# Performance work log

Measured on AMD Instinct MI355X. Metric: run time of the kernel, lower is better.

## Reference

```python
import jax, jax.numpy as jnp
import numpy as np

H = 1024          # hidden_size
NH = 16           # num_attention_heads
HD = H // NH      # head_size
EPS = 1e-5


def setup_inputs() -> dict:
    key = jax.random.key(0)
    ks = jax.random.split(key, 5)
    # xavier_uniform bound for Linear(in, out): sqrt(6/(in+out))
    b_qkv = float(np.sqrt(6.0 / (H + 3 * H)))
    b_out = float(np.sqrt(6.0 / (H + H)))
    return {
        "hidden_states": jax.random.normal(ks[0], (2, 2048, H), dtype=jnp.float32),
        "ln_gamma": jnp.ones((H,), jnp.float32),
        "ln_beta": jnp.zeros((H,), jnp.float32),
        "W_qkv": jax.random.uniform(ks[1], (3 * H, H), jnp.float32, -b_qkv, b_qkv),
        "b_qkv": jnp.zeros((3 * H,), jnp.float32),
        "W_out": jax.random.uniform(ks[2], (H, H), jnp.float32, -b_out, b_out),
        "b_out": jnp.zeros((H,), jnp.float32),
    }


def _attn_block(x, ln_gamma, ln_beta, W_qkv, b_qkv, W_out, b_out):
    B, S, _ = x.shape
    # Pre-LN
    mu = jnp.mean(x, axis=-1, keepdims=True)
    var = jnp.mean(jnp.square(x - mu), axis=-1, keepdims=True)
    xn = (x - mu) / jnp.sqrt(var + EPS) * ln_gamma + ln_beta
    # fused QKV projection: [B,S,3H]
    qkv = jnp.einsum("bsh,oh->bso", xn, W_qkv) + b_qkv
    qkv = qkv.reshape(B, S, 3, NH, HD).transpose(2, 0, 3, 1, 4)  # [3,B,NH,S,HD]
    q, k, v = qkv[0], qkv[1], qkv[2]
    scores = jnp.einsum("bhqd,bhkd->bhqk", q, k) / jnp.sqrt(jnp.asarray(HD, x.dtype))
    probs = jax.nn.softmax(scores, axis=-1)
    ctx = jnp.einsum("bhqk,bhkd->bhqd", probs, v)
    ctx = ctx.transpose(0, 2, 1, 3).reshape(B, S, H)
    out = jnp.einsum("bsh,oh->bso", ctx, W_out) + b_out  # dropout: eval mode = identity
    return x + out


def reference(hidden_states, ln_gamma, ln_beta, W_qkv, b_qkv, W_out, b_out):
    return _attn_block(hidden_states, ln_gamma, ln_beta, W_qkv, b_qkv, W_out, b_out)
```

## Files before the change

kernel.cpp:

```cpp
#include <hip/hip_runtime.h>
#include <stdint.h>

typedef unsigned short u16;
typedef __attribute__((ext_vector_type(8))) short bf16x8;
typedef __attribute__((ext_vector_type(4))) float f32x4;
typedef __attribute__((ext_vector_type(16))) float f32x16;
typedef __attribute__((ext_vector_type(4))) unsigned int u32x4;
typedef __attribute__((ext_vector_type(2))) unsigned int u32x2;
typedef __attribute__((ext_vector_type(4))) unsigned short u16x4;

#define QSCALE 0.18033688011112042f

typedef __attribute__((address_space(1))) const void gvoid;
typedef __attribute__((address_space(3))) void svoid;

__device__ __forceinline__ void cp16(const u16* g, u16* l) {
    __builtin_amdgcn_global_load_lds((gvoid*)g, (svoid*)l, 16, 0, 0);
}

__device__ __forceinline__ u16 f2bf(float f) {
    uint32_t u = __float_as_uint(f);
    u += 0x7fff + ((u >> 16) & 1);
    return (u16)(u >> 16);
}

__device__ __forceinline__ uint32_t pack_bf2(float lo, float hi) {
    uint32_t a = __float_as_uint(lo) + 0x8000u;
    uint32_t b = __float_as_uint(hi) + 0x8000u;
    return __builtin_amdgcn_perm(b, a, 0x07060302);
}

__device__ __forceinline__ f32x16 zero16() {
    f32x16 v;
    #pragma unroll
    for (int i = 0; i < 16; i++) v[i] = 0.f;
    return v;
}

__global__ __launch_bounds__(256) void k_pre(const float* __restrict__ X,
                                             const float* __restrict__ gam,
                                             const float* __restrict__ bet,
                                             u16* __restrict__ XN,
                                             const float* __restrict__ Wqkv, u16* __restrict__ Wq,
                                             const float* __restrict__ Wout, u16* __restrict__ Wo) {
    __shared__ float red[8];
    const int bid = blockIdx.x;
    if (bid < 4096) {
        int t = bid;
        const float4* xp = (const float4*)(X + (size_t)t * 1024);
        float4 x = xp[threadIdx.x];
        float s  = x.x + x.y + x.z + x.w;
        float s2 = x.x*x.x + x.y*x.y + x.z*x.z + x.w*x.w;
        #pragma unroll
        for (int off = 1; off < 64; off <<= 1) {
            s  += __shfl_xor(s,  off, 64);
            s2 += __shfl_xor(s2, off, 64);
        }
        int lane = threadIdx.x & 63, w = threadIdx.x >> 6;
        if (lane == 0) { red[w] = s; red[w + 4] = s2; }
        __syncthreads();
        s  = red[0] + red[1] + red[2] + red[3];
        s2 = red[4] + red[5] + red[6] + red[7];
        float mu  = s * (1.0f / 1024.0f);
        float var = s2 * (1.0f / 1024.0f) - mu * mu;
        float rin = rsqrtf(var + 1e-5f);
        float4 g = ((const float4*)gam)[threadIdx.x];
        float4 b = ((const float4*)bet)[threadIdx.x];
        u16x4 o;
        o.x = f2bf((x.x - mu) * rin * g.x + b.x);
        o.y = f2bf((x.y - mu) * rin * g.y + b.y);
        o.z = f2bf((x.z - mu) * rin * g.z + b.z);
        o.w = f2bf((x.w - mu) * rin * g.w + b.w);
        *(u16x4*)(XN + (size_t)t * 1024 + threadIdx.x * 4) = o;
    } else {
        int i = (bid - 4096) * 256 + threadIdx.x;
        const float* src; u16* dst;
        if (i < 786432) { src = Wqkv; dst = Wq; }
        else            { i -= 786432; src = Wout; dst = Wo; }
        float4 v = ((const float4*)src)[i];
        u16x4 o;
        o.x = f2bf(v.x); o.y = f2bf(v.y); o.z = f2bf(v.z); o.w = f2bf(v.w);
        ((u16x4*)dst)[i] = o;
    }
}

__device__ __forceinline__ void gemm_bt_tile(const u16* __restrict__ A, const u16* __restrict__ Bm,
                                             int m0, int n0, u16* As, u16* Bs, f32x4 acc[4][4]) {
    const int tid = threadIdx.x;
    const int lane = tid & 63;
    const int wv = tid >> 6;
    const int qi = lane & 15, g = lane >> 4, swz = qi & 7;
    const int wr = (wv >> 1) * 64, wc = (wv & 1) * 64;
    #pragma unroll
    for (int mi = 0; mi < 4; mi++)
        #pragma unroll
        for (int ni = 0; ni < 4; ni++) acc[mi][ni] = (f32x4){0.f, 0.f, 0.f, 0.f};

    const int row_in = tid >> 3;
    const int cs = (tid & 7) ^ (row_in & 7);
    for (int k0 = 0; k0 < 1024; k0 += 64) {
        __syncthreads();
        #pragma unroll
        for (int i = 0; i < 4; i++) {
            int row = i * 32 + row_in;
            cp16(A  + (size_t)(m0 + row) * 1024 + k0 + cs * 8, As + (i * 256 + wv * 64) * 8);
            cp16(Bm + (size_t)(n0 + row) * 1024 + k0 + cs * 8, Bs + (i * 256 + wv * 64) * 8);
        }
        __syncthreads();
        #pragma unroll
        for (int ks = 0; ks < 2; ks++) {
            bf16x8 af[4], bf[4];
            #pragma unroll
            for (int mi = 0; mi < 4; mi++)
                af[mi] = *(const bf16x8*)(As + (wr + mi * 16 + qi) * 64 + ((ks * 4 + g) ^ swz) * 8);
            #pragma unroll
            for (int ni = 0; ni < 4; ni++)
                bf[ni] = *(const bf16x8*)(Bs + (wc + ni * 16 + qi) * 64 + ((ks * 4 + g) ^ swz) * 8);
            #pragma unroll
            for (int mi = 0; mi < 4; mi++)
                #pragma unroll
                for (int ni = 0; ni < 4; ni++)
                    acc[mi][ni] = __builtin_amdgcn_mfma_f32_16x16x32_bf16(af[mi], bf[ni], acc[mi][ni], 0, 0, 0);
        }
    }
}


#define CFENCE asm volatile("" ::: "memory")
#define BARX() do { CFENCE; __builtin_amdgcn_s_barrier(); CFENCE; } while (0)
#define LGKM0() asm volatile("s_waitcnt lgkmcnt(0)" ::: "memory")

__global__ __launch_bounds__(512, 2) void k_qkv(const u16* __restrict__ XN, const u16* __restrict__ Wq,
                                                const float* __restrict__ bqkv,
                                                u16* __restrict__ Q, u16* __restrict__ K,
                                                u16* __restrict__ Vt) {
    __shared__ __align__(16) u16 SMEM[65536];
    const int tid = threadIdx.x;
    const int lane = tid & 63, w = tid >> 6;
    const int qi = lane & 15, g = lane >> 4, swz = qi & 7;
    const int wr = (w >> 2) * 128, wc = (w & 3) * 64;

    const int id = blockIdx.x;
    const int sw = (id & 7) * 24 + (id >> 3);
    const int n0 = (sw % 12) * 256;
    const int m0 = (sw / 12) * 256;

    const int laneRow = lane >> 3, laneCg = lane & 7;
    const int cs = laneCg ^ laneRow;
    const int aw = (w & 3) * 8 + (w >> 2) * 128;
    const u16* gA = XN + (size_t)(m0 + aw + laneRow) * 1024 + cs * 8;
    const u16* gB = Wq + (size_t)(n0 + w * 8 + laneRow) * 1024 + cs * 8;

#define SM_A(s) (SMEM + (s) * 32768)
#define SM_B(s) (SMEM + (s) * 32768 + 16384)
#define STAGE_A(tau, q, s) cp16(gA + (size_t)(q) * 32 * 1024 + (tau) * 64, SM_A(s) + ((q) * 32 + aw) * 64)
#define STAGE_B(tau, part, s)                                                                       \
    do { cp16(gB + (size_t)(part) * 128 * 1024 + (tau) * 64, SM_B(s) + ((part) * 128 + w * 8) * 64); \
         cp16(gB + (size_t)((part) * 128 + 64) * 1024 + (tau) * 64,                                  \
              SM_B(s) + ((part) * 128 + 64 + w * 8) * 64); } while (0)

    f32x4 acc[8][4];
    #pragma unroll
    for (int mi = 0; mi < 8; mi++)
        #pragma unroll
        for (int ni = 0; ni < 4; ni++) acc[mi][ni] = (f32x4){0.f, 0.f, 0.f, 0.f};
    bf16x8 bf[4][2];

    STAGE_B(0, 0, 0); STAGE_B(0, 1, 0);
    STAGE_A(0, 0, 0); STAGE_A(0, 1, 0); STAGE_A(0, 2, 0); STAGE_A(0, 3, 0);
    STAGE_B(1, 0, 1); STAGE_B(1, 1, 1);
    STAGE_A(1, 0, 1); STAGE_A(1, 1, 1);
    asm volatile("s_waitcnt vmcnt(6)" ::: "memory");
    BARX();

#define PHASE_A(q)                                                                                   \
    bf16x8 af[2][2];                                                                                 \
    _Pragma("unroll") for (int m2 = 0; m2 < 2; m2++)                                                 \
    _Pragma("unroll") for (int ks = 0; ks < 2; ks++)                                                 \
        af[m2][ks] = *(const bf16x8*)(as_ + (wr + ((q) * 2 + m2) * 16 + qi) * 64 + (((ks * 4 + g) ^ swz)) * 8);

#define DO_MFMA(q)                                                                                   \
    __builtin_amdgcn_s_setprio(1);                                                                   \
    _Pragma("unroll") for (int m2 = 0; m2 < 2; m2++)                                                 \
    _Pragma("unroll") for (int ni = 0; ni < 4; ni++) {                                               \
        acc[(q) * 2 + m2][ni] = __builtin_amdgcn_mfma_f32_16x16x32_bf16(af[m2][0], bf[ni][0], acc[(q) * 2 + m2][ni], 0, 0, 0); \
        acc[(q) * 2 + m2][ni] = __builtin_amdgcn_mfma_f32_16x16x32_bf16(af[m2][1], bf[ni][1], acc[(q) * 2 + m2][ni], 0, 0, 0); \
    }                                                                                                \
    __builtin_amdgcn_s_setprio(0);

    for (int t = 0; t < 16; t++) {
        const int s = t & 1;
        const u16* as_ = SM_A(s);
        const u16* bs_ = SM_B(s);
        {
            PHASE_A(0)
            #pragma unroll
            for (int ni = 0; ni < 4; ni++)
                #pragma unroll
                for (int ks = 0; ks < 2; ks++)
                    bf[ni][ks] = *(const bf16x8*)(bs_ + (wc + ni * 16 + qi) * 64 + ((ks * 4 + g) ^ swz) * 8);
            if (t < 15) { STAGE_A(t + 1, 2, s ^ 1); STAGE_A(t + 1, 3, s ^ 1); }
            BARX(); LGKM0();
            DO_MFMA(0)
            BARX();
        }
        {
            PHASE_A(1)
            if (t < 14) STAGE_B(t + 2, 0, s);
            BARX(); LGKM0();
            DO_MFMA(1)
            BARX();
        }
        {
            PHASE_A(2)
            if (t < 14) STAGE_B(t + 2, 1, s);
            BARX(); LGKM0();
            DO_MFMA(2)
            BARX();
        }
        {
            PHASE_A(3)
            if (t < 14) { STAGE_A(t + 2, 0, s); STAGE_A(t + 2, 1, s); }
            BARX(); LGKM0();
            DO_MFMA(3)
            if (t < 14) { asm volatile("s_waitcnt vmcnt(6)" ::: "memory"); }
            else        { asm volatile("s_waitcnt vmcnt(0)" ::: "memory"); }
            BARX();
        }
    }

    if (n0 < 2048) {
        const int which = n0 >> 10;
        u16* base = which ? K : Q;
        const float scale = which ? 1.0f : QSCALE;
        #pragma unroll
        for (int mi = 0; mi < 8; mi++)
            #pragma unroll
            for (int ni = 0; ni < 4; ni++)
                #pragma unroll
                for (int i = 0; i < 4; i++) {
                    int m = m0 + wr + mi * 16 + (g * 4 + i);
                    int n = n0 + wc + ni * 16 + qi;
                    float v = (acc[mi][ni][i] + bqkv[n]) * scale;
                    int b = m >> 11, ss = m & 2047;
                    int hh = (n >> 6) & 15, d = n & 63;
                    base[((size_t)(b * 16 + hh) * 2048 + ss) * 64 + d] = f2bf(v);
                }
    } else {
        u16* Tw = SMEM + w * 4352;
        const int head = (n0 + wc - 2048) >> 6;
        const int b = m0 >> 11;
        #pragma unroll
        for (int h = 0; h < 2; h++) {
            #pragma unroll
            for (int mi2 = 0; mi2 < 4; mi2++)
                #pragma unroll
                for (int ni = 0; ni < 4; ni++) {
                    int mi = h * 4 + mi2;
                    int n = n0 + wc + ni * 16 + qi;
                    float bq = bqkv[n];
                    u16x4 pk;
                    pk.x = f2bf(acc[mi][ni][0] + bq);
                    pk.y = f2bf(acc[mi][ni][1] + bq);
                    pk.z = f2bf(acc[mi][ni][2] + bq);
                    pk.w = f2bf(acc[mi][ni][3] + bq);
                    *(u16x4*)(Tw + (ni * 16 + qi) * 68 + mi2 * 16 + g * 4) = pk;
                }
            int s0 = (m0 + wr + h * 64) & 2047;
            u16* vrow = Vt + (size_t)(b * 16 + head) * 64 * 2048 + s0 + qi * 4;
            #pragma unroll
            for (int dd = 0; dd < 16; dd++) {
                int d = dd * 4 + g;
                u16x4 val = *(const u16x4*)(Tw + d * 68 + qi * 4);
                *(u16x4*)(vrow + (size_t)d * 2048) = val;
            }
        }
    }
#undef SM_A
#undef SM_B
#undef STAGE_A
#undef STAGE_B
#undef PHASE_A
#undef DO_MFMA
}

__global__ __launch_bounds__(256, 4) void k_attn(const u16* __restrict__ Q, const u16* __restrict__ K,
                                                 const u16* __restrict__ Vt, u16* __restrict__ CTX) {
    __shared__ __align__(16) u16 Ks[2][64 * 64];
    __shared__ __align__(16) u16 Vs[2][64 * 64];
    const int id = blockIdx.x;
    const int bh = (id & 7) * 4 + ((id >> 3) & 3);
    const int q0 = (id >> 5) * 64;
    const int lane = threadIdx.x & 63, w = threadIdx.x >> 6;
    const int l = lane & 31, h = lane >> 5;
    const int qg = w >> 1, kh = w & 1;
    const u16* Qp = Q  + (size_t)bh * (2048 * 64);
    const u16* Kp = K  + (size_t)bh * (2048 * 64);
    const u16* Vp = Vt + (size_t)bh * (64 * 2048);

    const int r0 = w * 8 + (lane >> 3);
    const int cs = (lane & 7) ^ (r0 & 7);
    const u16* kgp = Kp + (size_t)r0 * 64 + cs * 8;
    const u16* vgp = Vp + (size_t)r0 * 2048 + cs * 8;

    bf16x8 bq[4];
    {
        const u16* qb = Qp + (size_t)(q0 + qg * 32 + l) * 64 + h * 8;
        #pragma unroll
        for (int dk = 0; dk < 4; dk++) bq[dk] = *(const bf16x8*)(qb + dk * 16);
    }
    float ls = 0.f;
    f32x16 od0 = zero16(), od1 = zero16();

    cp16(kgp,              Ks[0] + w * 512);
    cp16(kgp + 32 * 64,    Ks[0] + w * 512 + 2048);
    cp16(vgp,              Vs[0] + w * 512);
    cp16(vgp + 32 * 2048,  Vs[0] + w * 512 + 2048);

    for (int t = 0; t < 32; ++t) {
        __syncthreads();
        if (t < 31) {
            const int nb = (t + 1) & 1;
            cp16(kgp + 4096,             Ks[nb] + w * 512);
            cp16(kgp + 4096 + 32 * 64,   Ks[nb] + w * 512 + 2048);
            cp16(vgp + 64,               Vs[nb] + w * 512);
            cp16(vgp + 64 + 32 * 2048,   Vs[nb] + w * 512 + 2048);
        }
        kgp += 4096; vgp += 64;
        const u16* ksp = Ks[t & 1];
        const u16* vsp = Vs[t & 1];

        f32x16 sv = zero16();
        __builtin_amdgcn_s_setprio(1);
        #pragma unroll
        for (int dk = 0; dk < 4; dk++) {
            bf16x8 ak = *(const bf16x8*)(ksp + (kh * 32 + l) * 64 + ((2 * dk + h) ^ (l & 7)) * 8);
            sv = __builtin_amdgcn_mfma_f32_32x32x16_bf16(ak, bq[dk], sv, 0, 0, 0);
        }
        __builtin_amdgcn_s_setprio(0);

        uint32_t y[2][4];
        #pragma unroll
        for (int s = 0; s < 4; s++)
            #pragma unroll
            for (int p = 0; p < 2; p++) {
                float e0 = __builtin_amdgcn_exp2f(sv[4 * s + 2 * p]);
                float e1 = __builtin_amdgcn_exp2f(sv[4 * s + 2 * p + 1]);
                ls += e0 + e1;
                y[p][s] = pack_bf2(e0, e1);
            }

        #pragma unroll
        for (int mt = 0; mt < 2; mt++) {
            u32x2 r0s = __builtin_amdgcn_permlane32_swap(y[0][2 * mt], y[0][2 * mt + 1], false, false);
            u32x2 r1s = __builtin_amdgcn_permlane32_swap(y[1][2 * mt], y[1][2 * mt + 1], false, false);
            u32x4 bw = {r0s.x, r1s.x, r0s.y, r1s.y};
            bf16x8 bp = *(const bf16x8*)&bw;
            bf16x8 av0 = *(const bf16x8*)(vsp + (l) * 64      + ((kh * 4 + 2 * mt + h) ^ (l & 7)) * 8);
            bf16x8 av1 = *(const bf16x8*)(vsp + (32 + l) * 64 + ((kh * 4 + 2 * mt + h) ^ (l & 7)) * 8);
            __builtin_amdgcn_s_setprio(1);
            od0 = __builtin_amdgcn_mfma_f32_32x32x16_bf16(av0, bp, od0, 0, 0, 0);
            od1 = __builtin_amdgcn_mfma_f32_32x32x16_bf16(av1, bp, od1, 0, 0, 0);
            __builtin_amdgcn_s_setprio(0);
        }
    }

    __syncthreads();
    float* cb  = (float*)&Ks[0][0];
    float* lsb = (float*)&Vs[0][0];
    if (kh == 1) {
        #pragma unroll
        for (int c = 0; c < 8; c++) {
            f32x4 v;
            if (c < 4) { v.x = od0[4*c+0]; v.y = od0[4*c+1]; v.z = od0[4*c+2]; v.w = od0[4*c+3]; }
            else       { v.x = od1[4*(c-4)+0]; v.y = od1[4*(c-4)+1]; v.z = od1[4*(c-4)+2]; v.w = od1[4*(c-4)+3]; }
            *(f32x4*)(cb + qg * 2048 + lane * 32 + (c ^ (lane & 7)) * 4) = v;
        }
        lsb[qg * 64 + lane] = ls;
    }
    __syncthreads();
    if (kh == 0) {
        #pragma unroll
        for (int c = 0; c < 8; c++) {
            f32x4 v = *(const f32x4*)(cb + qg * 2048 + lane * 32 + (c ^ (lane & 7)) * 4);
            if (c < 4) { od0[4*c+0] += v.x; od0[4*c+1] += v.y; od0[4*c+2] += v.z; od0[4*c+3] += v.w; }
            else       { od1[4*(c-4)+0] += v.x; od1[4*(c-4)+1] += v.y; od1[4*(c-4)+2] += v.z; od1[4*(c-4)+3] += v.w; }
        }
        ls += lsb[qg * 64 + lane];
        float lsum = ls + __shfl_xor(ls, 32, 64);
        float inv = 1.0f / lsum;
        const int b = bh >> 4, hh = bh & 15;
        size_t m = (size_t)b * 2048 + q0 + qg * 32 + l;
        u16* cp = CTX + m * 1024 + hh * 64;
        #pragma unroll
        for (int s = 0; s < 4; s++) {
            u16x4 o;
            o.x = f2bf(od0[4 * s + 0] * inv); o.y = f2bf(od0[4 * s + 1] * inv);
            o.z = f2bf(od0[4 * s + 2] * inv); o.w = f2bf(od0[4 * s + 3] * inv);
            *(u16x4*)(cp + 8 * s + 4 * h) = o;
            o.x = f2bf(od1[4 * s + 0] * inv); o.y = f2bf(od1[4 * s + 1] * inv);
            o.z = f2bf(od1[4 * s + 2] * inv); o.w = f2bf(od1[4 * s + 3] * inv);
            *(u16x4*)(cp + 32 + 8 * s + 4 * h) = o;
        }
    }
}

__global__ __launch_bounds__(256) void k_out(const u16* __restrict__ CTX, const u16* __restrict__ Wo,
                                             const float* __restrict__ bout, const float* __restrict__ X,
                                             float* __restrict__ OUT) {
    __shared__ __align__(16) u16 As[128 * 64], Bs[128 * 64];
    f32x4 acc[4][4];
    const int m0 = blockIdx.y * 128, n0 = blockIdx.x * 128;
    gemm_bt_tile(CTX, Wo, m0, n0, As, Bs, acc);
    const int lane = threadIdx.x & 63, wid = threadIdx.x >> 6;
    const int wr = (wid >> 1) * 64, wc = (wid & 1) * 64;
    #pragma unroll
    for (int mi = 0; mi < 4; mi++)
        #pragma unroll
        for (int ni = 0; ni < 4; ni++)
            #pragma unroll
            for (int i = 0; i < 4; i++) {
                size_t m = m0 + wr + mi * 16 + ((lane >> 4) * 4 + i);
                int n = n0 + wc + ni * 16 + (lane & 15);
                OUT[m * 1024 + n] = acc[mi][ni][i] + bout[n] + X[m * 1024 + n];
            }
}

extern "C" void kernel_launch(void* const* d_in, const int* in_sizes, int n_in,
                              void* d_out, int out_size, void* d_ws, size_t ws_size,
                              hipStream_t stream) {
    const float* X    = (const float*)d_in[0];
    const float* gam  = (const float*)d_in[1];
    const float* bet  = (const float*)d_in[2];
    const float* Wqkv = (const float*)d_in[3];
    const float* bqkv = (const float*)d_in[4];
    const float* Wout = (const float*)d_in[5];
    const float* bout = (const float*)d_in[6];
    float* OUT = (float*)d_out;

    u16* XN  = (u16*)d_ws;
    u16* Q   = XN  + (size_t)4 * 1024 * 1024;
    u16* K   = Q   + (size_t)4 * 1024 * 1024;
    u16* Vt  = K   + (size_t)4 * 1024 * 1024;
    u16* CTX = Vt  + (size_t)4 * 1024 * 1024;
    u16* Wq  = CTX + (size_t)4 * 1024 * 1024;
    u16* Wo  = Wq  + (size_t)3 * 1024 * 1024;

    k_pre<<<8192, 256, 0, stream>>>(X, gam, bet, XN, Wqkv, Wq, Wout, Wo);
    k_qkv<<<192, 512, 0, stream>>>(XN, Wq, bqkv, Q, K, Vt);
    k_attn<<<1024, 256, 0, stream>>>(Q, K, Vt, CTX);
    k_out<<<dim3(8, 32), 256, 0, stream>>>(CTX, Wo, bout, X, OUT);
}
```

Before: 193.9 us.

## Widen attention and output-projection blocks to 512 threads; use hardware bf16 pack

```diff
diff --git a/kernel.cpp b/kernel.cpp
--- a/kernel.cpp
+++ b/kernel.cpp
@@ -24,10 +24,10 @@
     return (u16)(u >> 16);
 }
 
-__device__ __forceinline__ uint32_t pack_bf2(float lo, float hi) {
-    uint32_t a = __float_as_uint(lo) + 0x8000u;
-    uint32_t b = __float_as_uint(hi) + 0x8000u;
-    return __builtin_amdgcn_perm(b, a, 0x07060302);
+__device__ __forceinline__ uint32_t cvtpk_bf2(float lo, float hi) {
+    uint32_t r;
+    asm("v_cvt_pk_bf16_f32 %0, %1, %2" : "=v"(r) : "v"(lo), "v"(hi));
+    return r;
 }
 
 __device__ __forceinline__ f32x16 zero16() {
@@ -84,47 +84,6 @@
     }
 }
 
-__device__ __forceinline__ void gemm_bt_tile(const u16* __restrict__ A, const u16* __restrict__ Bm,
-                                             int m0, int n0, u16* As, u16* Bs, f32x4 acc[4][4]) {
-    const int tid = threadIdx.x;
-    const int lane = tid & 63;
-    const int wv = tid >> 6;
-    const int qi = lane & 15, g = lane >> 4, swz = qi & 7;
-    const int wr = (wv >> 1) * 64, wc = (wv & 1) * 64;
-    #pragma unroll
-    for (int mi = 0; mi < 4; mi++)
-        #pragma unroll
-        for (int ni = 0; ni < 4; ni++) acc[mi][ni] = (f32x4){0.f, 0.f, 0.f, 0.f};
-
-    const int row_in = tid >> 3;
-    const int cs = (tid & 7) ^ (row_in & 7);
-    for (int k0 = 0; k0 < 1024; k0 += 64) {
-        __syncthreads();
-        #pragma unroll
-        for (int i = 0; i < 4; i++) {
-            int row = i * 32 + row_in;
-            cp16(A  + (size_t)(m0 + row) * 1024 + k0 + cs * 8, As + (i * 256 + wv * 64) * 8);
-            cp16(Bm + (size_t)(n0 + row) * 1024 + k0 + cs * 8, Bs + (i * 256 + wv * 64) * 8);
-        }
-        __syncthreads();
-        #pragma unroll
-        for (int ks = 0; ks < 2; ks++) {
-            bf16x8 af[4], bf[4];
-            #pragma unroll
-            for (int mi = 0; mi < 4; mi++)
-                af[mi] = *(const bf16x8*)(As + (wr + mi * 16 + qi) * 64 + ((ks * 4 + g) ^ swz) * 8);
-            #pragma unroll
-            for (int ni = 0; ni < 4; ni++)
-                bf[ni] = *(const bf16x8*)(Bs + (wc + ni * 16 + qi) * 64 + ((ks * 4 + g) ^ swz) * 8);
-            #pragma unroll
-            for (int mi = 0; mi < 4; mi++)
-                #pragma unroll
-                for (int ni = 0; ni < 4; ni++)
-                    acc[mi][ni] = __builtin_amdgcn_mfma_f32_16x16x32_bf16(af[mi], bf[ni], acc[mi][ni], 0, 0, 0);
-        }
-    }
-}
-
 
 #define CFENCE asm volatile("" ::: "memory")
 #define BARX() do { CFENCE; __builtin_amdgcn_s_barrier(); CFENCE; } while (0)
@@ -284,13 +243,15 @@
 #undef DO_MFMA
 }
 
-__global__ __launch_bounds__(256, 4) void k_attn(const u16* __restrict__ Q, const u16* __restrict__ K,
-                                                 const u16* __restrict__ Vt, u16* __restrict__ CTX) {
+__global__ __launch_bounds__(512) void k_attn(const u16* __restrict__ Q, const u16* __restrict__ K,
+                                              const u16* __restrict__ Vt, u16* __restrict__ CTX) {
     __shared__ __align__(16) u16 Ks[2][64 * 64];
     __shared__ __align__(16) u16 Vs[2][64 * 64];
+    __shared__ __align__(16) float CB[4][2048];
+    __shared__ float CBl[4][64];
     const int id = blockIdx.x;
     const int bh = (id & 7) * 4 + ((id >> 3) & 3);
-    const int q0 = (id >> 5) * 64;
+    const int q0 = (id >> 5) * 128;
     const int lane = threadIdx.x & 63, w = threadIdx.x >> 6;
     const int l = lane & 31, h = lane >> 5;
     const int qg = w >> 1, kh = w & 1;
@@ -300,8 +261,8 @@
 
     const int r0 = w * 8 + (lane >> 3);
     const int cs = (lane & 7) ^ (r0 & 7);
-    const u16* kgp = Kp + (size_t)r0 * 64 + cs * 8;
-    const u16* vgp = Vp + (size_t)r0 * 2048 + cs * 8;
+    const u16* kg = Kp + (size_t)r0 * 64 + cs * 8;
+    const u16* vg = Vp + (size_t)r0 * 2048 + cs * 8;
 
     bf16x8 bq[4];
     {
@@ -312,21 +273,16 @@
     float ls = 0.f;
     f32x16 od0 = zero16(), od1 = zero16();
 
-    cp16(kgp,              Ks[0] + w * 512);
-    cp16(kgp + 32 * 64,    Ks[0] + w * 512 + 2048);
-    cp16(vgp,              Vs[0] + w * 512);
-    cp16(vgp + 32 * 2048,  Vs[0] + w * 512 + 2048);
+    cp16(kg, Ks[0] + w * 512);
+    cp16(vg, Vs[0] + w * 512);
 
     for (int t = 0; t < 32; ++t) {
         __syncthreads();
         if (t < 31) {
-            const int nb = (t + 1) & 1;
-            cp16(kgp + 4096,             Ks[nb] + w * 512);
-            cp16(kgp + 4096 + 32 * 64,   Ks[nb] + w * 512 + 2048);
-            cp16(vgp + 64,               Vs[nb] + w * 512);
-            cp16(vgp + 64 + 32 * 2048,   Vs[nb] + w * 512 + 2048);
-        }
-        kgp += 4096; vgp += 64;
+            cp16(kg + 4096, Ks[(t + 1) & 1] + w * 512);
+            cp16(vg + 64,   Vs[(t + 1) & 1] + w * 512);
+        }
+        kg += 4096; vg += 64;
         const u16* ksp = Ks[t & 1];
         const u16* vsp = Vs[t & 1];
 
@@ -347,7 +303,7 @@
                 float e0 = __builtin_amdgcn_exp2f(sv[4 * s + 2 * p]);
                 float e1 = __builtin_amdgcn_exp2f(sv[4 * s + 2 * p + 1]);
                 ls += e0 + e1;
-                y[p][s] = pack_bf2(e0, e1);
+                y[p][s] = cvtpk_bf2(e0, e1);
             }
 
         #pragma unroll
@@ -365,9 +321,8 @@
         }
     }
 
+    float* cb = &CB[0][0];
     __syncthreads();
-    float* cb  = (float*)&Ks[0][0];
-    float* lsb = (float*)&Vs[0][0];
     if (kh == 1) {
         #pragma unroll
         for (int c = 0; c < 8; c++) {
@@ -376,7 +331,7 @@
             else       { v.x = od1[4*(c-4)+0]; v.y = od1[4*(c-4)+1]; v.z = od1[4*(c-4)+2]; v.w = od1[4*(c-4)+3]; }
             *(f32x4*)(cb + qg * 2048 + lane * 32 + (c ^ (lane & 7)) * 4) = v;
         }
-        lsb[qg * 64 + lane] = ls;
+        CBl[qg][lane] = ls;
     }
     __syncthreads();
     if (kh == 0) {
@@ -386,7 +341,7 @@
             if (c < 4) { od0[4*c+0] += v.x; od0[4*c+1] += v.y; od0[4*c+2] += v.z; od0[4*c+3] += v.w; }
             else       { od1[4*(c-4)+0] += v.x; od1[4*(c-4)+1] += v.y; od1[4*(c-4)+2] += v.z; od1[4*(c-4)+3] += v.w; }
         }
-        ls += lsb[qg * 64 + lane];
+        ls += CBl[qg][lane];
         float lsum = ls + __shfl_xor(ls, 32, 64);
         float inv = 1.0f / lsum;
         const int b = bh >> 4, hh = bh & 15;
@@ -405,23 +360,61 @@
     }
 }
 
-__global__ __launch_bounds__(256) void k_out(const u16* __restrict__ CTX, const u16* __restrict__ Wo,
+__global__ __launch_bounds__(512) void k_out(const u16* __restrict__ CTX, const u16* __restrict__ Wo,
                                              const float* __restrict__ bout, const float* __restrict__ X,
                                              float* __restrict__ OUT) {
     __shared__ __align__(16) u16 As[128 * 64], Bs[128 * 64];
-    f32x4 acc[4][4];
+    const int tid = threadIdx.x;
+    const int lane = tid & 63;
+    const int wv = tid >> 6;
+    const int qi = lane & 15, g = lane >> 4, swz = qi & 7;
+    const int wr = (wv >> 1) * 32, wc = (wv & 1) * 64;
     const int m0 = blockIdx.y * 128, n0 = blockIdx.x * 128;
-    gemm_bt_tile(CTX, Wo, m0, n0, As, Bs, acc);
-    const int lane = threadIdx.x & 63, wid = threadIdx.x >> 6;
-    const int wr = (wid >> 1) * 64, wc = (wid & 1) * 64;
+
+    f32x4 acc[2][4];
     #pragma unroll
-    for (int mi = 0; mi < 4; mi++)
+    for (int mi = 0; mi < 2; mi++)
+        #pragma unroll
+        for (int ni = 0; ni < 4; ni++) acc[mi][ni] = (f32x4){0.f, 0.f, 0.f, 0.f};
+
+    const int row_in = tid >> 3;
+    const int cs = (tid & 7) ^ (row_in & 7);
+    for (int k0 = 0; k0 < 1024; k0 += 64) {
+        __syncthreads();
+        #pragma unroll
+        for (int i = 0; i < 2; i++) {
+            int row = i * 64 + row_in;
+            cp16(CTX + (size_t)(m0 + row) * 1024 + k0 + cs * 8, As + (i * 512 + wv * 64) * 8);
+            cp16(Wo  + (size_t)(n0 + row) * 1024 + k0 + cs * 8, Bs + (i * 512 + wv * 64) * 8);
+        }
+        __syncthreads();
+        #pragma unroll
+        for (int ks = 0; ks < 2; ks++) {
+            bf16x8 af[2], bf[4];
+            #pragma unroll
+            for (int mi = 0; mi < 2; mi++)
+                af[mi] = *(const bf16x8*)(As + (wr + mi * 16 + qi) * 64 + ((ks * 4 + g) ^ swz) * 8);
+            #pragma unroll
+            for (int ni = 0; ni < 4; ni++)
+                bf[ni] = *(const bf16x8*)(Bs + (wc + ni * 16 + qi) * 64 + ((ks * 4 + g) ^ swz) * 8);
+            __builtin_amdgcn_s_setprio(1);
+            #pragma unroll
+            for (int mi = 0; mi < 2; mi++)
+                #pragma unroll
+                for (int ni = 0; ni < 4; ni++)
+                    acc[mi][ni] = __builtin_amdgcn_mfma_f32_16x16x32_bf16(af[mi], bf[ni], acc[mi][ni], 0, 0, 0);
+            __builtin_amdgcn_s_setprio(0);
+        }
+    }
+
+    #pragma unroll
+    for (int mi = 0; mi < 2; mi++)
         #pragma unroll
         for (int ni = 0; ni < 4; ni++)
             #pragma unroll
             for (int i = 0; i < 4; i++) {
-                size_t m = m0 + wr + mi * 16 + ((lane >> 4) * 4 + i);
-                int n = n0 + wc + ni * 16 + (lane & 15);
+                size_t m = m0 + wr + mi * 16 + (g * 4 + i);
+                int n = n0 + wc + ni * 16 + qi;
                 OUT[m * 1024 + n] = acc[mi][ni][i] + bout[n] + X[m * 1024 + n];
             }
 }
@@ -448,6 +441,6 @@
 
     k_pre<<<8192, 256, 0, stream>>>(X, gam, bet, XN, Wqkv, Wq, Wout, Wo);
     k_qkv<<<192, 512, 0, stream>>>(XN, Wq, bqkv, Q, K, Vt);
-    k_attn<<<1024, 256, 0, stream>>>(Q, K, Vt, CTX);
-    k_out<<<dim3(8, 32), 256, 0, stream>>>(CTX, Wo, bout, X, OUT);
-}
+    k_attn<<<512, 512, 0, stream>>>(Q, K, Vt, CTX);
+    k_out<<<dim3(8, 32), 512, 0, stream>>>(CTX, Wo, bout, X, OUT);
+}
```

Result: faster. 182.8 us (-5.7%).
